# Optimization experiments

Measured on AMD Instinct MI355X. Metric: run time of the kernel, lower is better.

Reference implementation:

```python
import jax, jax.numpy as jnp
import numpy as np

K = 16          # knn size (init kwarg k)
BN_EPS = 1e-5


def _batchnorm(x, gamma, beta):
    # x: [B, M, C]; torch BatchNorm2d train-mode stats over (batch, spatial) per channel
    mu = jnp.mean(x, axis=(0, 1), keepdims=True)
    var = jnp.var(x, axis=(0, 1), keepdims=True)
    return (x - mu) * jax.lax.rsqrt(var + BN_EPS) * gamma + beta


def _gather_neighbors(values, idx):
    # values: [B, N, C], idx: [B, M, K] -> [B, M, K, C]
    return jax.vmap(lambda v, i: v[i])(values, idx)


def setup_inputs() -> dict:
    key = jax.random.key(0)
    ks = jax.random.split(key, 6)
    B, N, C, P, O = 8, 2048, 128, 3, 256
    Cin = C + P  # in_feat_dim = 131
    x = jax.random.normal(ks[0], (B, N, C), jnp.float32)
    pos = jax.random.uniform(ks[1], (B, N, P), jnp.float32)
    W1 = jax.random.normal(ks[2], (Cin, O), jnp.float32) * (1.0 / np.sqrt(Cin))
    b1 = jnp.zeros((O,), jnp.float32)
    g1 = jnp.ones((O,), jnp.float32)
    be1 = jnp.zeros((O,), jnp.float32)
    W2 = jax.random.normal(ks[3], (O, O), jnp.float32) * (1.0 / np.sqrt(O))
    b2 = jnp.zeros((O,), jnp.float32)
    g2 = jnp.ones((O,), jnp.float32)
    be2 = jnp.zeros((O,), jnp.float32)
    return {"x": x, "pos": pos, "W1": W1, "b1": b1, "g1": g1, "be1": be1,
            "W2": W2, "b2": b2, "g2": g2, "be2": be2}


def reference(x, pos, W1, b1, g1, be1, W2, b2, g2, be2):
    # sampled_idx=None -> sampled set == all N points; relative_pos=False
    # Pairwise squared distances [B, N, N] (the duplicate unused `dist` is dead code, omitted)
    d = jnp.sum((pos[:, :, None, :] - pos[:, None, :, :]) ** 2, axis=-1)
    # topk smallest distances -> neighbor indices [B, N, K]
    _, nn_idx = jax.lax.top_k(-d, K)
    gathered_pos = _gather_neighbors(pos, nn_idx)          # [B, N, K, 3]
    gathered_x = _gather_neighbors(x, nn_idx)              # [B, N, K, C]
    gathered_feat = jnp.concatenate([gathered_x, gathered_pos], axis=-1)  # [B, N, K, C+3]
    avg = jnp.mean(gathered_feat, axis=2)                  # [B, N, C+3]  (mean over K, keepdim then squeezed)
    # conv2d 1x1 + BN + ReLU, then conv2d 1x1 + BN (last_act=False)
    h = jax.nn.relu(_batchnorm(jnp.einsum("bnc,co->bno", avg, W1) + b1, g1, be1))
    out = _batchnorm(jnp.einsum("bnc,co->bno", h, W2) + b2, g2, be2)
    return out  # [B, N, out_feat_dim]
```

## Files before the change

kernel.cpp:

```cpp
#include <hip/hip_runtime.h>
#include <hip/hip_bf16.h>

namespace {

constexpr int BB = 8;
constexpr int NPTS = 2048;
constexpr int CC = 128;
constexpr int MM = BB * NPTS;
constexpr int OO = 256;
constexpr int K1 = 160;
constexpr int KNNK = 16;

typedef __attribute__((ext_vector_type(8))) short bf16x8;
typedef __attribute__((ext_vector_type(8))) unsigned short u16x8;
typedef __attribute__((ext_vector_type(4))) float f32x4;

__device__ __forceinline__ unsigned short f2bf(float v) {
  unsigned u = __builtin_bit_cast(unsigned, v);
  u += 0x7FFFu + ((u >> 16) & 1u);
  return (unsigned short)(u >> 16);
}

__device__ __forceinline__ float bf2f(unsigned short s) {
  unsigned u = (unsigned)s << 16;
  return __builtin_bit_cast(float, u);
}

__device__ __forceinline__ unsigned long long shflxor64(unsigned long long v, int m) {
  int lo = __shfl_xor((int)(unsigned)v, m, 64);
  int hi = __shfl_xor((int)(unsigned)(v >> 32), m, 64);
  return ((unsigned long long)(unsigned)hi << 32) | (unsigned)lo;
}

template <int J>
__device__ __forceinline__ unsigned long long partner64(unsigned long long v) {
  int lo = (int)(unsigned)v, hi = (int)(unsigned)(v >> 32);
  int plo, phi;
  if constexpr (J == 1) {
    plo = __builtin_amdgcn_mov_dpp(lo, 0xB1, 0xF, 0xF, true);
    phi = __builtin_amdgcn_mov_dpp(hi, 0xB1, 0xF, 0xF, true);
  } else if constexpr (J == 2) {
    plo = __builtin_amdgcn_mov_dpp(lo, 0x4E, 0xF, 0xF, true);
    phi = __builtin_amdgcn_mov_dpp(hi, 0x4E, 0xF, 0xF, true);
  } else if constexpr (J == 4) {
    plo = __builtin_amdgcn_ds_swizzle(lo, 0x101F);
    phi = __builtin_amdgcn_ds_swizzle(hi, 0x101F);
  } else if constexpr (J == 8) {
    plo = __builtin_amdgcn_ds_swizzle(lo, 0x201F);
    phi = __builtin_amdgcn_ds_swizzle(hi, 0x201F);
  } else if constexpr (J == 16) {
    plo = __builtin_amdgcn_ds_swizzle(lo, 0x401F);
    phi = __builtin_amdgcn_ds_swizzle(hi, 0x401F);
  } else {
    plo = __shfl_xor(lo, 32, 64);
    phi = __shfl_xor(hi, 32, 64);
  }
  return ((unsigned long long)(unsigned)phi << 32) | (unsigned)plo;
}

__device__ __forceinline__ unsigned long long bitonic_sort64(unsigned long long key, int lane) {
#define BSTAGE(K, J)                                                        \
  {                                                                         \
    unsigned long long o = partner64<J>(key);                               \
    bool keepMin = (((lane & (K)) == 0) == ((lane & (J)) == 0));            \
    bool less = key < o;                                                    \
    key = (less == keepMin) ? key : o;                                      \
  }
  BSTAGE(2, 1)
  BSTAGE(4, 2) BSTAGE(4, 1)
  BSTAGE(8, 4) BSTAGE(8, 2) BSTAGE(8, 1)
  BSTAGE(16, 8) BSTAGE(16, 4) BSTAGE(16, 2) BSTAGE(16, 1)
  BSTAGE(32, 16) BSTAGE(32, 8) BSTAGE(32, 4) BSTAGE(32, 2) BSTAGE(32, 1)
  BSTAGE(64, 32) BSTAGE(64, 16) BSTAGE(64, 8) BSTAGE(64, 4) BSTAGE(64, 2) BSTAGE(64, 1)
#undef BSTAGE
  return key;
}

__device__ __forceinline__ unsigned long long u64min(unsigned long long a, unsigned long long b) {
  return a < b ? a : b;
}

__global__ __launch_bounds__(256, 6) void knn_kernel(const float* __restrict__ pos,
                                                     int* __restrict__ nn_idx) {
#pragma clang fp contract(off)
  __shared__ float2 pxy[NPTS];
  __shared__ float pzz[NPTS];
  __shared__ unsigned long long sbuf[4][64];
  const int b = blockIdx.y;
  const int tid = threadIdx.x;
  const float* pb = pos + (size_t)b * NPTS * 3;
  for (int i = tid; i < NPTS; i += 256) {
    pxy[i] = make_float2(pb[3 * i], pb[3 * i + 1]);
    pzz[i] = pb[3 * i + 2];
  }
  __syncthreads();
  const int lane = tid & 63;
  const int wid = tid >> 6;
  const int q = blockIdx.x * 4 + wid;
  const float2 qxy = pxy[q];
  const float qz = pzz[q];

  float dvals[32];
  unsigned long long mink = ~0ull;
#pragma unroll
  for (int t = 0; t < 32; ++t) {
    const int j = lane + (t << 6);
    float2 pp = pxy[j];
    float dx = qxy.x - pp.x;
    float dy = qxy.y - pp.y;
    float dz = qz - pzz[j];
    float d = ((dx * dx) + (dy * dy)) + (dz * dz);
    dvals[t] = d;
    unsigned long long key = ((unsigned long long)__float_as_uint(d) << 11) | (unsigned)j;
    mink = u64min(mink, key);
  }
  unsigned long long skey = bitonic_sort64(mink, lane);
  unsigned Tlo = (unsigned)__builtin_amdgcn_readlane((int)(unsigned)skey, 15);
  unsigned Thi = (unsigned)__builtin_amdgcn_readlane((int)(unsigned)(skey >> 32), 15);
  const unsigned long long Tkey = ((unsigned long long)Thi << 32) | Tlo;

  unsigned long long* buf = sbuf[wid];
  int base = 0;
#pragma unroll
  for (int t = 0; t < 32; ++t) {
    unsigned long long key =
        ((unsigned long long)__float_as_uint(dvals[t]) << 11) | (unsigned)(lane + (t << 6));
    bool surv = key <= Tkey;
    unsigned long long mask = __ballot(surv);
    if (surv) {
      int off = __popcll(mask & ((1ull << lane) - 1ull));
      if (base + off < 64) buf[base + off] = key;
    }
    base += (int)__popcll(mask);
  }

  int* out = nn_idx + ((size_t)b * NPTS + q) * KNNK;
  if (base <= 64) {
    unsigned long long key = (lane < base) ? buf[lane] : ~0ull;
    key = bitonic_sort64(key, lane);
    if (lane < 16) out[lane] = (int)(key & 2047ull);
  } else {
    unsigned long long prev = 0;
    for (int o = 0; o < 16; ++o) {
      unsigned long long m = ~0ull;
#pragma unroll
      for (int t = 0; t < 32; ++t) {
        unsigned long long key =
            ((unsigned long long)__float_as_uint(dvals[t]) << 11) | (unsigned)(lane + (t << 6));
        if (o == 0 || key > prev) m = u64min(m, key);
      }
#pragma unroll
      for (int off = 32; off > 0; off >>= 1) m = u64min(m, shflxor64(m, off));
      if (lane == 0) out[o] = (int)(m & 2047ull);
      prev = m;
    }
  }
}

__global__ __launch_bounds__(256) void gather_prep(const float* __restrict__ x,
                                                   const float* __restrict__ pos,
                                                   const int* __restrict__ nn_idx,
                                                   unsigned short* __restrict__ avg,
                                                   const float* __restrict__ W1,
                                                   const float* __restrict__ W2,
                                                   unsigned short* __restrict__ W1T,
                                                   unsigned short* __restrict__ W2T,
                                                   double* __restrict__ stats) {
  const int tid = threadIdx.x;
  if (blockIdx.x >= MM / 4) {
    const int i2 = blockIdx.x - MM / 4;
    if (i2 == 208) {
      for (int i = tid; i < 1024; i += 256) stats[i] = 0.0;
      return;
    }
    const int i = i2 * 512 + (tid << 1);
#pragma unroll
    for (int e = 0; e < 2; ++e) {
      const int ii = i + e;
      if (ii < 256 * K1) {
        const int n = ii / K1, k = ii - n * K1;
        W1T[ii] = f2bf(k < 131 ? W1[k * 256 + n] : 0.f);
      } else {
        const int j = ii - 256 * K1;
        const int n = j >> 8, k = j & 255;
        W2T[j] = f2bf(W2[k * 256 + n]);
      }
    }
    return;
  }
  const int lane = tid & 63;
  const int wid = tid >> 6;
  const int p = blockIdx.x * 4 + wid;
  const int b = p >> 11;
  const int* ip = nn_idx + (size_t)p * KNNK;
  int idx[16];
#pragma unroll
  for (int k = 0; k < 16; ++k) idx[k] = ip[k];
  const float* xb = x + (size_t)b * NPTS * CC;
  float ax = 0.f, ay = 0.f;
#pragma unroll
  for (int k = 0; k < 16; ++k) {
    float2 v = *(const float2*)(xb + (size_t)idx[k] * CC + lane * 2);
    ax += v.x;
    ay += v.y;
  }
  unsigned short h0 = f2bf(ax * 0.0625f);
  unsigned short h1 = f2bf(ay * 0.0625f);
  *(unsigned*)(avg + (size_t)p * K1 + lane * 2) = (unsigned)h0 | ((unsigned)h1 << 16);
  if (lane < 32) {
    unsigned short o = 0;
    if (lane < 3) {
      const float* pb = pos + (size_t)b * NPTS * 3;
      float v = 0.f;
#pragma unroll
      for (int k = 0; k < 16; ++k) v += pb[idx[k] * 3 + lane];
      o = f2bf(v * 0.0625f);
    }
    avg[(size_t)p * K1 + 128 + lane] = o;
  }
}

template <bool BN_IN>
__global__ __launch_bounds__(256) void gemm_stats(
    const unsigned short* __restrict__ A, const unsigned short* __restrict__ BT,
    const float* __restrict__ bias,
    const double* __restrict__ dsumIn, const double* __restrict__ dsumsqIn,
    const float* __restrict__ gIn, const float* __restrict__ beIn,
    double* __restrict__ dsum, double* __restrict__ dsumsq,
    unsigned short* __restrict__ pre, int Kp) {
  __shared__ __align__(16) unsigned short As[64][56];
  __shared__ __align__(16) unsigned short Bs[64][56];
  __shared__ float sSum[64], sSq[64];
  __shared__ float sScA[256], sShA[256];
  const int tid = threadIdx.x;
  if (tid < 64) { sSum[tid] = 0.f; sSq[tid] = 0.f; }
  if constexpr (BN_IN) {
    double mu = dsumIn[tid] * (1.0 / 16384.0);
    double var = dsumsqIn[tid] * (1.0 / 16384.0) - mu * mu;
    float sc = (float)((double)gIn[tid] / sqrt(var + 1e-5));
    sScA[tid] = sc;
    sShA[tid] = beIn[tid] - (float)mu * sc;
    __syncthreads();
  }
  const int m0 = blockIdx.x * 64;
  const int n0 = blockIdx.y * 64;
  const int w = tid >> 6, lane = tid & 63;
  const int wr = w >> 1, wc = w & 1;
  const int l15 = lane & 15;
  const int g = lane >> 4;
  const int kk = g * 8;
  f32x4 acc[2][2] = {};
  const int sr = tid >> 2;
  const int sk = (tid & 3) * 8;
  const unsigned short* Aptr = A + (size_t)(m0 + sr) * Kp + sk;
  const unsigned short* Bptr = BT + (size_t)(n0 + sr) * Kp + sk;
  for (int k0 = 0; k0 < Kp; k0 += 32) {
    if constexpr (BN_IN) {
      u16x8 a = *(const u16x8*)(Aptr + k0);
      u16x8 ta;
#pragma unroll
      for (int e = 0; e < 8; ++e) {
        const int col = k0 + sk + e;
        float v = fmaf(bf2f(a[e]), sScA[col], sShA[col]);
        ta[e] = f2bf(fmaxf(v, 0.f));
      }
      *(u16x8*)(&As[sr][sk]) = ta;
    } else {
      *(int4*)(&As[sr][sk]) = *(const int4*)(Aptr + k0);
    }
    *(int4*)(&Bs[sr][sk]) = *(const int4*)(Bptr + k0);
    __syncthreads();
    bf16x8 a0  = *(const bf16x8*)(&As[wr * 32 + l15][kk]);
    bf16x8 a1  = *(const bf16x8*)(&As[wr * 32 + 16 + l15][kk]);
    bf16x8 b0  = *(const bf16x8*)(&Bs[wc * 32 + l15][kk]);
    bf16x8 b1v = *(const bf16x8*)(&Bs[wc * 32 + 16 + l15][kk]);
    acc[0][0] = __builtin_amdgcn_mfma_f32_16x16x32_bf16(a0, b0,  acc[0][0], 0, 0, 0);
    acc[0][1] = __builtin_amdgcn_mfma_f32_16x16x32_bf16(a0, b1v, acc[0][1], 0, 0, 0);
    acc[1][0] = __builtin_amdgcn_mfma_f32_16x16x32_bf16(a1, b0,  acc[1][0], 0, 0, 0);
    acc[1][1] = __builtin_amdgcn_mfma_f32_16x16x32_bf16(a1, b1v, acc[1][1], 0, 0, 0);
    __syncthreads();
  }

  float s[2] = {0.f, 0.f}, q2[2] = {0.f, 0.f};
  unsigned short vb[2][2][4];
#pragma unroll
  for (int fc = 0; fc < 2; ++fc) {
    float bv = bias[n0 + wc * 32 + fc * 16 + l15];
#pragma unroll
    for (int fr = 0; fr < 2; ++fr)
#pragma unroll
      for (int r = 0; r < 4; ++r) {
        float xv = acc[fr][fc][r] + bv;
        unsigned short h = f2bf(xv);
        vb[fr][fc][r] = h;
        float xq = bf2f(h);
        s[fc] += xq;
        q2[fc] = fmaf(xq, xq, q2[fc]);
      }
  }
#pragma unroll
  for (int fc = 0; fc < 2; ++fc) {
    s[fc] += __shfl_xor(s[fc], 16, 64);
    s[fc] += __shfl_xor(s[fc], 32, 64);
    q2[fc] += __shfl_xor(q2[fc], 16, 64);
    q2[fc] += __shfl_xor(q2[fc], 32, 64);
  }
  if (lane < 16) {
#pragma unroll
    for (int fc = 0; fc < 2; ++fc) {
      atomicAdd(&sSum[wc * 32 + fc * 16 + lane], s[fc]);
      atomicAdd(&sSq[wc * 32 + fc * 16 + lane], q2[fc]);
    }
  }
#pragma unroll
  for (int fc = 0; fc < 2; ++fc) {
    int col = n0 + wc * 32 + fc * 16 + l15;
#pragma unroll
    for (int fr = 0; fr < 2; ++fr)
#pragma unroll
      for (int r = 0; r < 4; ++r) {
        int row = m0 + wr * 32 + fr * 16 + g * 4 + r;
        pre[(size_t)row * OO + col] = vb[fr][fc][r];
      }
  }
  __syncthreads();
  if (tid < 64) {
    atomicAdd(&dsum[n0 + tid], (double)sSum[tid]);
    atomicAdd(&dsumsq[n0 + tid], (double)sSq[tid]);
  }
}

__global__ __launch_bounds__(256) void bn_apply(const unsigned short* __restrict__ pre,
                                                const double* __restrict__ dsum,
                                                const double* __restrict__ dsumsq,
                                                const float* __restrict__ gamma,
                                                const float* __restrict__ beta,
                                                float* __restrict__ outp) {
  __shared__ float sSc[256], sSh[256];
  const int tid = threadIdx.x;
  {
    double mu = dsum[tid] * (1.0 / 16384.0);
    double var = dsumsq[tid] * (1.0 / 16384.0) - mu * mu;
    float sc = (float)((double)gamma[tid] / sqrt(var + 1e-5));
    sSc[tid] = sc;
    sSh[tid] = beta[tid] - (float)mu * sc;
  }
  __syncthreads();
  const int cg = (tid & 31) * 8;
  float sc[8], sh[8];
#pragma unroll
  for (int j = 0; j < 8; ++j) { sc[j] = sSc[cg + j]; sh[j] = sSh[cg + j]; }
  const int r0 = blockIdx.x * 32 + (tid >> 5);
#pragma unroll
  for (int it = 0; it < 4; ++it) {
    const int row = r0 + it * 8;
    u16x8 v = *(const u16x8*)(pre + (size_t)row * OO + cg);
    float4 o0, o1;
    o0.x = fmaf(bf2f(v[0]), sc[0], sh[0]);
    o0.y = fmaf(bf2f(v[1]), sc[1], sh[1]);
    o0.z = fmaf(bf2f(v[2]), sc[2], sh[2]);
    o0.w = fmaf(bf2f(v[3]), sc[3], sh[3]);
    o1.x = fmaf(bf2f(v[4]), sc[4], sh[4]);
    o1.y = fmaf(bf2f(v[5]), sc[5], sh[5]);
    o1.z = fmaf(bf2f(v[6]), sc[6], sh[6]);
    o1.w = fmaf(bf2f(v[7]), sc[7], sh[7]);
    float* op = outp + (size_t)row * OO + cg;
    *(float4*)op = o0;
    *(float4*)(op + 4) = o1;
  }
}

}

extern "C" void kernel_launch(void* const* d_in, const int* in_sizes, int n_in,
                              void* d_out, int out_size, void* d_ws, size_t ws_size,
                              hipStream_t stream) {
  const float* x   = (const float*)d_in[0];
  const float* pos = (const float*)d_in[1];
  const float* W1  = (const float*)d_in[2];
  const float* b1  = (const float*)d_in[3];
  const float* g1  = (const float*)d_in[4];
  const float* be1 = (const float*)d_in[5];
  const float* W2  = (const float*)d_in[6];
  const float* b2  = (const float*)d_in[7];
  const float* g2  = (const float*)d_in[8];
  const float* be2 = (const float*)d_in[9];

  char* ws = (char*)d_ws;
  double* stats        = (double*)(ws + 0);
  int* nn_idx          = (int*)(ws + 12288);
  unsigned short* avg  = (unsigned short*)(ws + 1060864);
  unsigned short* W1T  = (unsigned short*)(ws + 6303744);
  unsigned short* W2T  = (unsigned short*)(ws + 6385664);
  unsigned short* pre1 = (unsigned short*)(ws + 6516736);
  unsigned short* pre2 = (unsigned short*)(ws + 14905344);

  knn_kernel<<<dim3(NPTS / 4, BB), 256, 0, stream>>>(pos, nn_idx);
  gather_prep<<<MM / 4 + 209, 256, 0, stream>>>(x, pos, nn_idx, avg, W1, W2, W1T, W2T, stats);
  gemm_stats<false><<<dim3(MM / 64, OO / 64), 256, 0, stream>>>(
      avg, W1T, b1, nullptr, nullptr, nullptr, nullptr,
      stats, stats + 256, pre1, K1);
  gemm_stats<true><<<dim3(MM / 64, OO / 64), 256, 0, stream>>>(
      pre1, W2T, b2, stats, stats + 256, g1, be1,
      stats + 512, stats + 768, pre2, OO);
  bn_apply<<<MM / 32, 256, 0, stream>>>(pre2, stats + 512, stats + 768, g2, be2, (float*)d_out);
}
```

Before: 84.46 us.

## Fuse KNN selection with neighbor gather and weight prep into one kernel

```diff
diff --git a/kernel.cpp b/kernel.cpp
--- a/kernel.cpp
+++ b/kernel.cpp
@@ -9,7 +9,7 @@
 constexpr int MM = BB * NPTS;
 constexpr int OO = 256;
 constexpr int K1 = 160;
-constexpr int KNNK = 16;
+constexpr int NKNN = MM / 4;
 
 typedef __attribute__((ext_vector_type(8))) short bf16x8;
 typedef __attribute__((ext_vector_type(8))) unsigned short u16x8;
@@ -80,95 +80,20 @@
   return a < b ? a : b;
 }
 
-__global__ __launch_bounds__(256, 6) void knn_kernel(const float* __restrict__ pos,
-                                                     int* __restrict__ nn_idx) {
+__global__ __launch_bounds__(256, 6) void knn_gather(const float* __restrict__ pos,
+                                                     const float* __restrict__ x,
+                                                     unsigned short* __restrict__ avg,
+                                                     const float* __restrict__ W1,
+                                                     const float* __restrict__ W2,
+                                                     unsigned short* __restrict__ W1T,
+                                                     unsigned short* __restrict__ W2T,
+                                                     double* __restrict__ stats) {
 #pragma clang fp contract(off)
   __shared__ float2 pxy[NPTS];
-  __shared__ float pzz[NPTS];
   __shared__ unsigned long long sbuf[4][64];
-  const int b = blockIdx.y;
   const int tid = threadIdx.x;
-  const float* pb = pos + (size_t)b * NPTS * 3;
-  for (int i = tid; i < NPTS; i += 256) {
-    pxy[i] = make_float2(pb[3 * i], pb[3 * i + 1]);
-    pzz[i] = pb[3 * i + 2];
-  }
-  __syncthreads();
-  const int lane = tid & 63;
-  const int wid = tid >> 6;
-  const int q = blockIdx.x * 4 + wid;
-  const float2 qxy = pxy[q];
-  const float qz = pzz[q];
-
-  float dvals[32];
-  unsigned long long mink = ~0ull;
-#pragma unroll
-  for (int t = 0; t < 32; ++t) {
-    const int j = lane + (t << 6);
-    float2 pp = pxy[j];
-    float dx = qxy.x - pp.x;
-    float dy = qxy.y - pp.y;
-    float dz = qz - pzz[j];
-    float d = ((dx * dx) + (dy * dy)) + (dz * dz);
-    dvals[t] = d;
-    unsigned long long key = ((unsigned long long)__float_as_uint(d) << 11) | (unsigned)j;
-    mink = u64min(mink, key);
-  }
-  unsigned long long skey = bitonic_sort64(mink, lane);
-  unsigned Tlo = (unsigned)__builtin_amdgcn_readlane((int)(unsigned)skey, 15);
-  unsigned Thi = (unsigned)__builtin_amdgcn_readlane((int)(unsigned)(skey >> 32), 15);
-  const unsigned long long Tkey = ((unsigned long long)Thi << 32) | Tlo;
-
-  unsigned long long* buf = sbuf[wid];
-  int base = 0;
-#pragma unroll
-  for (int t = 0; t < 32; ++t) {
-    unsigned long long key =
-        ((unsigned long long)__float_as_uint(dvals[t]) << 11) | (unsigned)(lane + (t << 6));
-    bool surv = key <= Tkey;
-    unsigned long long mask = __ballot(surv);
-    if (surv) {
-      int off = __popcll(mask & ((1ull << lane) - 1ull));
-      if (base + off < 64) buf[base + off] = key;
-    }
-    base += (int)__popcll(mask);
-  }
-
-  int* out = nn_idx + ((size_t)b * NPTS + q) * KNNK;
-  if (base <= 64) {
-    unsigned long long key = (lane < base) ? buf[lane] : ~0ull;
-    key = bitonic_sort64(key, lane);
-    if (lane < 16) out[lane] = (int)(key & 2047ull);
-  } else {
-    unsigned long long prev = 0;
-    for (int o = 0; o < 16; ++o) {
-      unsigned long long m = ~0ull;
-#pragma unroll
-      for (int t = 0; t < 32; ++t) {
-        unsigned long long key =
-            ((unsigned long long)__float_as_uint(dvals[t]) << 11) | (unsigned)(lane + (t << 6));
-        if (o == 0 || key > prev) m = u64min(m, key);
-      }
-#pragma unroll
-      for (int off = 32; off > 0; off >>= 1) m = u64min(m, shflxor64(m, off));
-      if (lane == 0) out[o] = (int)(m & 2047ull);
-      prev = m;
-    }
-  }
-}
-
-__global__ __launch_bounds__(256) void gather_prep(const float* __restrict__ x,
-                                                   const float* __restrict__ pos,
-                                                   const int* __restrict__ nn_idx,
-                                                   unsigned short* __restrict__ avg,
-                                                   const float* __restrict__ W1,
-                                                   const float* __restrict__ W2,
-                                                   unsigned short* __restrict__ W1T,
-                                                   unsigned short* __restrict__ W2T,
-                                                   double* __restrict__ stats) {
-  const int tid = threadIdx.x;
-  if (blockIdx.x >= MM / 4) {
-    const int i2 = blockIdx.x - MM / 4;
+  if (blockIdx.x >= NKNN) {
+    const int i2 = blockIdx.x - NKNN;
     if (i2 == 208) {
       for (int i = tid; i < 1024; i += 256) stats[i] = 0.0;
       return;
@@ -188,35 +113,98 @@
     }
     return;
   }
+  const int b = blockIdx.x >> 9;
+  const float* pb = pos + (size_t)b * NPTS * 3;
+  for (int i = tid; i < NPTS; i += 256) {
+    pxy[i] = make_float2(pb[3 * i], pb[3 * i + 1]);
+  }
+  __syncthreads();
   const int lane = tid & 63;
   const int wid = tid >> 6;
-  const int p = blockIdx.x * 4 + wid;
-  const int b = p >> 11;
-  const int* ip = nn_idx + (size_t)p * KNNK;
-  int idx[16];
-#pragma unroll
-  for (int k = 0; k < 16; ++k) idx[k] = ip[k];
+  const int q = ((blockIdx.x & 511) << 2) + wid;
+  const float2 qxy = pxy[q];
+  const float qz = pb[3 * q + 2];
+
+  float dvals[32];
+  unsigned long long mink = ~0ull;
+#pragma unroll
+  for (int t = 0; t < 32; ++t) {
+    const int j = lane + (t << 6);
+    float2 pp = pxy[j];
+    float pz = pb[3 * j + 2];
+    float dx = qxy.x - pp.x;
+    float dy = qxy.y - pp.y;
+    float dz = qz - pz;
+    float d = ((dx * dx) + (dy * dy)) + (dz * dz);
+    dvals[t] = d;
+    unsigned long long key = ((unsigned long long)__float_as_uint(d) << 11) | (unsigned)j;
+    mink = u64min(mink, key);
+  }
+  unsigned long long skey = bitonic_sort64(mink, lane);
+  unsigned Tlo = (unsigned)__builtin_amdgcn_readlane((int)(unsigned)skey, 15);
+  unsigned Thi = (unsigned)__builtin_amdgcn_readlane((int)(unsigned)(skey >> 32), 15);
+  const unsigned long long Tkey = ((unsigned long long)Thi << 32) | Tlo;
+
+  unsigned long long* buf = sbuf[wid];
+  int base = 0;
+#pragma unroll
+  for (int t = 0; t < 32; ++t) {
+    unsigned long long key =
+        ((unsigned long long)__float_as_uint(dvals[t]) << 11) | (unsigned)(lane + (t << 6));
+    bool surv = key <= Tkey;
+    unsigned long long mask = __ballot(surv);
+    if (surv) {
+      int off = __popcll(mask & ((1ull << lane) - 1ull));
+      if (base + off < 64) buf[base + off] = key;
+    }
+    base += (int)__popcll(mask);
+  }
+
+  int myidx = 0;
+  if (base <= 64) {
+    unsigned long long key = (lane < base) ? buf[lane] : ~0ull;
+    key = bitonic_sort64(key, lane);
+    if (lane < 16) myidx = (int)(key & 2047ull);
+  } else {
+    unsigned long long prev = 0;
+    for (int o = 0; o < 16; ++o) {
+      unsigned long long m = ~0ull;
+#pragma unroll
+      for (int t = 0; t < 32; ++t) {
+        unsigned long long key =
+            ((unsigned long long)__float_as_uint(dvals[t]) << 11) | (unsigned)(lane + (t << 6));
+        if (o == 0 || key > prev) m = u64min(m, key);
+      }
+#pragma unroll
+      for (int off = 32; off > 0; off >>= 1) m = u64min(m, shflxor64(m, off));
+      if (lane == o) myidx = (int)(m & 2047ull);
+      prev = m;
+    }
+  }
+
   const float* xb = x + (size_t)b * NPTS * CC;
   float ax = 0.f, ay = 0.f;
+  int idxs[16];
 #pragma unroll
   for (int k = 0; k < 16; ++k) {
-    float2 v = *(const float2*)(xb + (size_t)idx[k] * CC + lane * 2);
+    idxs[k] = __builtin_amdgcn_readlane(myidx, k);
+    float2 v = *(const float2*)(xb + (size_t)idxs[k] * CC + lane * 2);
     ax += v.x;
     ay += v.y;
   }
+  const size_t p = (size_t)b * NPTS + q;
   unsigned short h0 = f2bf(ax * 0.0625f);
   unsigned short h1 = f2bf(ay * 0.0625f);
-  *(unsigned*)(avg + (size_t)p * K1 + lane * 2) = (unsigned)h0 | ((unsigned)h1 << 16);
+  *(unsigned*)(avg + p * K1 + lane * 2) = (unsigned)h0 | ((unsigned)h1 << 16);
   if (lane < 32) {
     unsigned short o = 0;
     if (lane < 3) {
-      const float* pb = pos + (size_t)b * NPTS * 3;
       float v = 0.f;
 #pragma unroll
-      for (int k = 0; k < 16; ++k) v += pb[idx[k] * 3 + lane];
+      for (int k = 0; k < 16; ++k) v += pb[idxs[k] * 3 + lane];
       o = f2bf(v * 0.0625f);
     }
-    avg[(size_t)p * K1 + 128 + lane] = o;
+    avg[p * K1 + 128 + lane] = o;
   }
 }
 
@@ -388,15 +376,13 @@
 
   char* ws = (char*)d_ws;
   double* stats        = (double*)(ws + 0);
-  int* nn_idx          = (int*)(ws + 12288);
   unsigned short* avg  = (unsigned short*)(ws + 1060864);
   unsigned short* W1T  = (unsigned short*)(ws + 6303744);
   unsigned short* W2T  = (unsigned short*)(ws + 6385664);
   unsigned short* pre1 = (unsigned short*)(ws + 6516736);
   unsigned short* pre2 = (unsigned short*)(ws + 14905344);
 
-  knn_kernel<<<dim3(NPTS / 4, BB), 256, 0, stream>>>(pos, nn_idx);
-  gather_prep<<<MM / 4 + 209, 256, 0, stream>>>(x, pos, nn_idx, avg, W1, W2, W1T, W2T, stats);
+  knn_gather<<<NKNN + 209, 256, 0, stream>>>(pos, x, avg, W1, W2, W1T, W2T, stats);
   gemm_stats<false><<<dim3(MM / 64, OO / 64), 256, 0, stream>>>(
       avg, W1T, b1, nullptr, nullptr, nullptr, nullptr,
       stats, stats + 256, pre1, K1);
```

Measured after the change: 83.68 us. No clear change (-0.9%).
